# Performance work log

Hardware: AMD Instinct MI355X
Metric: run time of the kernel (lower is better)

The kernel has to match this reference:

```python
import jax, jax.numpy as jnp
import numpy as np

N = 2048      # factor dims (d_in == units == N)
K = 16        # nonzeros per row of each factor
B = 16384     # batch
F = 3         # number of sparse factors
NNZ = N * K


def _pattern(f):
    # Fixed, compile-time-known structured sparsity pattern (butterfly-like):
    # row r has nonzeros at cols (r + k*(N//K) + f) % N, k in [0, K)
    r = np.repeat(np.arange(N), K)
    k = np.tile(np.arange(K), N)
    c = (r + k * (N // K) + f) % N
    return r.astype(np.int32), c.astype(np.int32)


def setup_inputs() -> dict:
    key = jax.random.key(0)
    kx, k0, k1, k2, ks, kb = jax.random.split(key, 6)
    # glorot-ish scale for sparse factor values: fan ~ K nonzeros per row
    wscale = (2.0 / (K + K)) ** 0.5
    rows0, cols0 = _pattern(0)
    rows1, cols1 = _pattern(1)
    rows2, cols2 = _pattern(2)
    return {
        "x": jax.random.normal(kx, (B, N), dtype=jnp.float32),
        "vals0": jax.random.normal(k0, (NNZ,), dtype=jnp.float32) * wscale,
        "vals1": jax.random.normal(k1, (NNZ,), dtype=jnp.float32) * wscale,
        "vals2": jax.random.normal(k2, (NNZ,), dtype=jnp.float32) * wscale,
        "rows0": jnp.asarray(rows0), "cols0": jnp.asarray(cols0),
        "rows1": jnp.asarray(rows1), "cols1": jnp.asarray(cols1),
        "rows2": jnp.asarray(rows2), "cols2": jnp.asarray(cols2),
        "scaling": jax.random.uniform(ks, (1,), dtype=jnp.float32, minval=0.5, maxval=1.5),
        "bias": jax.random.normal(kb, (N,), dtype=jnp.float32) * 0.02,
    }


def _dense_factor(vals, rows, cols):
    # materialize the sparse factor (values scattered into the fixed pattern)
    return jnp.zeros((N, N), dtype=vals.dtype).at[rows, cols].set(vals)


def reference(x, vals0, vals1, vals2, rows0, cols0, rows1, cols1, rows2, cols2, scaling, bias):
    # output = relu(scaling * (x @ W0 @ W1 @ W2) + bias)
    y = x
    for vals, rows, cols in ((vals0, rows0, cols0), (vals1, rows1, cols1), (vals2, rows2, cols2)):
        y = y @ _dense_factor(vals, rows, cols)  # [B, N]
    y = scaling * y + bias
    return jax.nn.relu(y)
```

## Files before the change

kernel.cpp:

```cpp
#include <hip/hip_runtime.h>

#define NN 2048
#define KK 16

__global__ __launch_bounds__(128) void sfd_compose(const float* __restrict__ v0,
                                                   const float* __restrict__ v1,
                                                   const float* __restrict__ v2,
                                                   const float* __restrict__ scaling,
                                                   float* __restrict__ mcl) {
  int tid = blockIdx.x * 128 + threadIdx.x;
  int c = tid >> 4;
  int i = tid & 15;

  int A  = (c + NN - 3) & (NN - 1);
  int s1 = A & 127;
  int T0 = A >> 7;
  int rx = s1 + (i << 7);

  float vr[16];
#pragma unroll
  for (int m = 0; m < 16; ++m)
    vr[m] = v0[rx * 16 + ((T0 - i - m) & 15)];

  float acc = 0.f;
#pragma unroll 4
  for (int k2 = 0; k2 < 16; ++k2) {
    int r1 = (c + NN - 2 - (k2 << 7)) & (NN - 1);
    int cm = (r1 + NN - 1) & (NN - 1);
    float w = 0.f;
#pragma unroll
    for (int k1 = 0; k1 < 16; ++k1) {
      int r0 = (cm - (k1 << 7)) & (NN - 1);
      w = fmaf(v1[r0 * 16 + k1], vr[(k1 + k2) & 15], w);
    }
    acc = fmaf(v2[r1 * 16 + k2], w, acc);
  }
  int s = c & 127;
  int j = c >> 7;
  mcl[(s * 16 + j) * 16 + i] = acc * scaling[0];
}

__device__ __forceinline__ void sfd_loadq(float4 (&pf)[4], const float* __restrict__ x,
                                          int rb, int w0, int t) {
#pragma unroll
  for (int q = 0; q < 4; ++q) {
    int idx = t + (q << 8);
    int uu = idx & 31;
    int ig = (idx >> 5) & 3;
    int rr = idx >> 7;
    const float* xrow = x + (size_t)(rb + rr) * NN;
    int cb = w0 + uu + (ig << 9);
    pf[q].x = xrow[cb & (NN - 1)];
    pf[q].y = xrow[(cb + 128) & (NN - 1)];
    pf[q].z = xrow[(cb + 256) & (NN - 1)];
    pf[q].w = xrow[(cb + 384) & (NN - 1)];
  }
}

__device__ __forceinline__ void sfd_writeq(const float4 (&pf)[4], float* xs, int t) {
#pragma unroll
  for (int q = 0; q < 4; ++q) {
    int idx = t + (q << 8);
    int uu = idx & 31;
    int ig = (idx >> 5) & 3;
    int rr = idx >> 7;
    *(float4*)(xs + (rr * 32 + uu) * 20 + (ig << 2)) = pf[q];
  }
}

__device__ __forceinline__ void sfd_compute(const float* xs, int u,
                                            const float (&mc0)[16], const float (&mc1)[16],
                                            float bi0, float bi1,
                                            int rb, int c0, int c1,
                                            float* __restrict__ out) {
#pragma unroll 1
  for (int r = 0; r < 8; ++r) {
    const float4* xr = (const float4*)(xs + (r * 32 + u) * 20);
    float xv[16];
    *(float4*)(xv + 0)  = xr[0];
    *(float4*)(xv + 4)  = xr[1];
    *(float4*)(xv + 8)  = xr[2];
    *(float4*)(xv + 12) = xr[3];
    float acc0 = bi0, acc1 = bi1;
#pragma unroll
    for (int i = 0; i < 16; ++i) {
      acc0 = fmaf(xv[i], mc0[i], acc0);
      acc1 = fmaf(xv[i], mc1[i], acc1);
    }
    size_t ob = (size_t)(rb + r) * NN;
    __builtin_nontemporal_store(fmaxf(acc0, 0.f), &out[ob + c0]);
    __builtin_nontemporal_store(fmaxf(acc1, 0.f), &out[ob + c1]);
  }
}

__global__ __launch_bounds__(256, 4) void sfd_apply(const float* __restrict__ x,
                                                    const float* __restrict__ mcl,
                                                    const float* __restrict__ bias,
                                                    float* __restrict__ out) {
  const int S0 = blockIdx.x << 5;
  const int b0 = blockIdx.y << 5;
  const int t = threadIdx.x;
  const int u = t & 31;
  const int jp = t >> 5;
  const int s = S0 + u;
  const int j0 = jp << 1;
  const int w0 = (S0 + 125) & 127;
  const int shift = (w0 + u) >> 7;

  float mc0[16], mc1[16];
  {
    const float* r0p = mcl + ((s * 16 + j0) << 4);
#pragma unroll
    for (int i = 0; i < 16; ++i) {
      int ic = (i + shift) & 15;
      mc0[i] = r0p[ic];
      mc1[i] = r0p[16 + ic];
    }
  }
  const int c0 = s + (j0 << 7);
  const int c1 = c0 + 128;
  const float bi0 = bias[c0];
  const float bi1 = bias[c1];

  __shared__ float xs[2][8 * 32 * 20];

  float4 pfA[4], pfB[4];

  sfd_loadq(pfA, x, b0 + 0,  w0, t);
  sfd_writeq(pfA, xs[0], t);
  sfd_loadq(pfB, x, b0 + 8,  w0, t);
  __syncthreads();

  sfd_compute(xs[0], u, mc0, mc1, bi0, bi1, b0 + 0,  c0, c1, out);
  sfd_writeq(pfB, xs[1], t);
  sfd_loadq(pfA, x, b0 + 16, w0, t);
  __syncthreads();

  sfd_compute(xs[1], u, mc0, mc1, bi0, bi1, b0 + 8,  c0, c1, out);
  sfd_writeq(pfA, xs[0], t);
  sfd_loadq(pfB, x, b0 + 24, w0, t);
  __syncthreads();

  sfd_compute(xs[0], u, mc0, mc1, bi0, bi1, b0 + 16, c0, c1, out);
  sfd_writeq(pfB, xs[1], t);
  __syncthreads();

  sfd_compute(xs[1], u, mc0, mc1, bi0, bi1, b0 + 24, c0, c1, out);
}

extern "C" void kernel_launch(void* const* d_in, const int* in_sizes, int n_in,
                              void* d_out, int out_size, void* d_ws, size_t ws_size,
                              hipStream_t stream) {
  const float* x       = (const float*)d_in[0];
  const float* v0      = (const float*)d_in[1];
  const float* v1      = (const float*)d_in[2];
  const float* v2      = (const float*)d_in[3];
  const float* scaling = (const float*)d_in[10];
  const float* bias    = (const float*)d_in[11];
  float* out = (float*)d_out;

  float* mcl = (float*)d_ws;

  const int B = in_sizes[0] / NN;

  hipLaunchKernelGGL(sfd_compose, dim3(256), dim3(128), 0, stream, v0, v1, v2, scaling, mcl);
  hipLaunchKernelGGL(sfd_apply, dim3(4, B >> 5), dim3(256), 0, stream, x, mcl, bias, out);
}
```

Baseline: 268.2 us.

## Restructure apply kernel to load full x rows with coalesced float4 reads

Each block of the apply kernel now covers 32 batch rows across all 2048 output columns with 512 threads, so it stages whole contiguous x rows into shared memory using coalesced float4 loads. This replaces the earlier strided, wrapped scalar gathers. Each thread now keeps four composed column vectors and produces four outputs per row. The change drops the register double-buffering between load and compute and uses a 64 KB shared buffer, which may limit occupancy and expose load latency.

```diff
diff --git a/kernel.cpp b/kernel.cpp
--- a/kernel.cpp
+++ b/kernel.cpp
@@ -40,112 +40,71 @@
   mcl[(s * 16 + j) * 16 + i] = acc * scaling[0];
 }
 
-__device__ __forceinline__ void sfd_loadq(float4 (&pf)[4], const float* __restrict__ x,
-                                          int rb, int w0, int t) {
-#pragma unroll
-  for (int q = 0; q < 4; ++q) {
-    int idx = t + (q << 8);
-    int uu = idx & 31;
-    int ig = (idx >> 5) & 3;
-    int rr = idx >> 7;
-    const float* xrow = x + (size_t)(rb + rr) * NN;
-    int cb = w0 + uu + (ig << 9);
-    pf[q].x = xrow[cb & (NN - 1)];
-    pf[q].y = xrow[(cb + 128) & (NN - 1)];
-    pf[q].z = xrow[(cb + 256) & (NN - 1)];
-    pf[q].w = xrow[(cb + 384) & (NN - 1)];
-  }
-}
-
-__device__ __forceinline__ void sfd_writeq(const float4 (&pf)[4], float* xs, int t) {
-#pragma unroll
-  for (int q = 0; q < 4; ++q) {
-    int idx = t + (q << 8);
-    int uu = idx & 31;
-    int ig = (idx >> 5) & 3;
-    int rr = idx >> 7;
-    *(float4*)(xs + (rr * 32 + uu) * 20 + (ig << 2)) = pf[q];
-  }
-}
-
-__device__ __forceinline__ void sfd_compute(const float* xs, int u,
-                                            const float (&mc0)[16], const float (&mc1)[16],
-                                            float bi0, float bi1,
-                                            int rb, int c0, int c1,
-                                            float* __restrict__ out) {
-#pragma unroll 1
-  for (int r = 0; r < 8; ++r) {
-    const float4* xr = (const float4*)(xs + (r * 32 + u) * 20);
-    float xv[16];
-    *(float4*)(xv + 0)  = xr[0];
-    *(float4*)(xv + 4)  = xr[1];
-    *(float4*)(xv + 8)  = xr[2];
-    *(float4*)(xv + 12) = xr[3];
-    float acc0 = bi0, acc1 = bi1;
-#pragma unroll
-    for (int i = 0; i < 16; ++i) {
-      acc0 = fmaf(xv[i], mc0[i], acc0);
-      acc1 = fmaf(xv[i], mc1[i], acc1);
-    }
-    size_t ob = (size_t)(rb + r) * NN;
-    __builtin_nontemporal_store(fmaxf(acc0, 0.f), &out[ob + c0]);
-    __builtin_nontemporal_store(fmaxf(acc1, 0.f), &out[ob + c1]);
-  }
-}
-
-__global__ __launch_bounds__(256, 4) void sfd_apply(const float* __restrict__ x,
+__global__ __launch_bounds__(512, 4) void sfd_apply(const float* __restrict__ x,
                                                     const float* __restrict__ mcl,
                                                     const float* __restrict__ bias,
                                                     float* __restrict__ out) {
-  const int S0 = blockIdx.x << 5;
-  const int b0 = blockIdx.y << 5;
-  const int t = threadIdx.x;
-  const int u = t & 31;
-  const int jp = t >> 5;
-  const int s = S0 + u;
-  const int j0 = jp << 1;
-  const int w0 = (S0 + 125) & 127;
-  const int shift = (w0 + u) >> 7;
+  const int t  = threadIdx.x;
+  const int u  = t & 127;
+  const int g  = t >> 7;
+  const int rb = blockIdx.x << 5;
+  const int W  = (u + 125) & 127;
 
-  float mc0[16], mc1[16];
+  float mc[4][16];
   {
-    const float* r0p = mcl + ((s * 16 + j0) << 4);
+    const float4* mp = (const float4*)(mcl + (size_t)u * 256 + (size_t)g * 64);
 #pragma unroll
-    for (int i = 0; i < 16; ++i) {
-      int ic = (i + shift) & 15;
-      mc0[i] = r0p[ic];
-      mc1[i] = r0p[16 + ic];
+    for (int q = 0; q < 16; ++q) {
+      float4 v = mp[q];
+      mc[q >> 2][(q & 3) * 4 + 0] = v.x;
+      mc[q >> 2][(q & 3) * 4 + 1] = v.y;
+      mc[q >> 2][(q & 3) * 4 + 2] = v.z;
+      mc[q >> 2][(q & 3) * 4 + 3] = v.w;
     }
   }
-  const int c0 = s + (j0 << 7);
-  const int c1 = c0 + 128;
-  const float bi0 = bias[c0];
-  const float bi1 = bias[c1];
+  const int cb = u + (g << 9);
+  float bi[4];
+#pragma unroll
+  for (int jj = 0; jj < 4; ++jj) bi[jj] = bias[cb + (jj << 7)];
 
-  __shared__ float xs[2][8 * 32 * 20];
+  __shared__ float xs[8 * 2048];
 
-  float4 pfA[4], pfB[4];
-
-  sfd_loadq(pfA, x, b0 + 0,  w0, t);
-  sfd_writeq(pfA, xs[0], t);
-  sfd_loadq(pfB, x, b0 + 8,  w0, t);
-  __syncthreads();
-
-  sfd_compute(xs[0], u, mc0, mc1, bi0, bi1, b0 + 0,  c0, c1, out);
-  sfd_writeq(pfB, xs[1], t);
-  sfd_loadq(pfA, x, b0 + 16, w0, t);
-  __syncthreads();
-
-  sfd_compute(xs[1], u, mc0, mc1, bi0, bi1, b0 + 8,  c0, c1, out);
-  sfd_writeq(pfA, xs[0], t);
-  sfd_loadq(pfB, x, b0 + 24, w0, t);
-  __syncthreads();
-
-  sfd_compute(xs[0], u, mc0, mc1, bi0, bi1, b0 + 16, c0, c1, out);
-  sfd_writeq(pfB, xs[1], t);
-  __syncthreads();
-
-  sfd_compute(xs[1], u, mc0, mc1, bi0, bi1, b0 + 24, c0, c1, out);
+  for (int ch = 0; ch < 4; ++ch) {
+    const float4* xc = (const float4*)(x + ((size_t)(rb + (ch << 3)) << 11));
+    {
+      float4 pf[4];
+#pragma unroll
+      for (int q = 0; q < 4; ++q) pf[q] = xc[t + (q << 9)];
+#pragma unroll
+      for (int q = 0; q < 4; ++q) ((float4*)xs)[t + (q << 9)] = pf[q];
+#pragma unroll
+      for (int q = 0; q < 4; ++q) pf[q] = xc[t + ((q + 4) << 9)];
+#pragma unroll
+      for (int q = 0; q < 4; ++q) ((float4*)xs)[t + ((q + 4) << 9)] = pf[q];
+    }
+    __syncthreads();
+#pragma unroll 1
+    for (int r = 0; r < 8; ++r) {
+      const float* xr = xs + (r << 11) + W;
+      float xv[16];
+#pragma unroll
+      for (int i = 0; i < 16; ++i) xv[i] = xr[i << 7];
+      float a0 = bi[0], a1 = bi[1], a2 = bi[2], a3 = bi[3];
+#pragma unroll
+      for (int i = 0; i < 16; ++i) {
+        a0 = fmaf(xv[i], mc[0][i], a0);
+        a1 = fmaf(xv[i], mc[1][i], a1);
+        a2 = fmaf(xv[i], mc[2][i], a2);
+        a3 = fmaf(xv[i], mc[3][i], a3);
+      }
+      size_t ob = ((size_t)(rb + (ch << 3) + r) << 11) + cb;
+      __builtin_nontemporal_store(fmaxf(a0, 0.f), &out[ob]);
+      __builtin_nontemporal_store(fmaxf(a1, 0.f), &out[ob + 128]);
+      __builtin_nontemporal_store(fmaxf(a2, 0.f), &out[ob + 256]);
+      __builtin_nontemporal_store(fmaxf(a3, 0.f), &out[ob + 384]);
+    }
+    __syncthreads();
+  }
 }
 
 extern "C" void kernel_launch(void* const* d_in, const int* in_sizes, int n_in,
@@ -164,5 +123,5 @@
   const int B = in_sizes[0] / NN;
 
   hipLaunchKernelGGL(sfd_compose, dim3(256), dim3(128), 0, stream, v0, v1, v2, scaling, mcl);
-  hipLaunchKernelGGL(sfd_apply, dim3(4, B >> 5), dim3(256), 0, stream, x, mcl, bias, out);
+  hipLaunchKernelGGL(sfd_apply, dim3(B >> 5), dim3(512), 0, stream, x, mcl, bias, out);
 }
```

Result: no change. 269.1 us (+0.3%).
